# Kernel tuning notes

Hardware: AMD Instinct MI355X
Metric: run time of the kernel (lower is better)

## Reference

```python
import jax, jax.numpy as jnp
import numpy as np

B, N, F_IN, H, FO = 4, 2048, 256, 4, 64


def setup_inputs() -> dict:
    key = jax.random.key(0)
    k1, k2, k3, k4, k5 = jax.random.split(key, 5)
    x = jax.random.normal(k1, (B, N, F_IN), dtype=jnp.float32)
    # random 0/1 adjacency with self-loops so every row of softmax is finite
    adj = jax.random.randint(k2, (N, N), 0, 2).astype(jnp.float32)
    adj = jnp.maximum(adj, jnp.eye(N, dtype=jnp.float32))
    # parameters (xavier-uniform style)
    lim_w = float(np.sqrt(6.0 / (F_IN + H * FO)))
    W = jax.random.uniform(k3, (F_IN, H * FO), minval=-lim_w, maxval=lim_w, dtype=jnp.float32)
    lim_a = float(np.sqrt(6.0 / (H + FO)))
    a_src = jax.random.uniform(k4, (H, FO), minval=-lim_a, maxval=lim_a, dtype=jnp.float32)
    a_dst = jax.random.uniform(k5, (H, FO), minval=-lim_a, maxval=lim_a, dtype=jnp.float32)
    return {"x": x, "adj": adj, "W": W, "a_src": a_src, "a_dst": a_dst}


def reference(x, adj, W, a_src, a_dst):
    # h: (B, N, H, FO)
    h = (x @ W).reshape(B, N, H, FO)
    attn_src = jnp.einsum("bnhf,hf->bnh", h, a_src)  # (B,N,H)
    attn_dst = jnp.einsum("bnhf,hf->bnh", h, a_dst)  # (B,N,H)
    # scores[b,i,j,h] = src[b,i,h] + dst[b,j,h]
    scores = attn_src[:, :, None, :] + attn_dst[:, None, :, :]
    scores = jax.nn.leaky_relu(scores, negative_slope=0.2)
    mask = (adj == 0)[None, :, :, None]  # (1,N,N,1)
    scores = jnp.where(mask, -jnp.inf, scores)
    attn = jax.nn.softmax(scores, axis=2)  # softmax over neighbors j
    # dropout is identity in eval mode / p=0
    out = jnp.einsum("bijh,bjhf->bihf", attn, h)  # (B,N,H,FO)
    return out.reshape(B, N, H * FO)  # concat=True
```

## Files before the change

kernel.cpp:

```cpp
#include <hip/hip_runtime.h>
#include <hip/hip_bf16.h>
#include <math.h>

#define B 4
#define N 2048
#define FIN 256
#define H 4
#define FO 64
#define M (B*N)
#define HF (H*FO)

typedef __attribute__((ext_vector_type(8))) short short8;
typedef __attribute__((ext_vector_type(4))) float float4v;
typedef __attribute__((ext_vector_type(4))) int int4v;

#if __has_builtin(__builtin_amdgcn_exp2f)
#define EXP2(x) __builtin_amdgcn_exp2f(x)
#else
#define EXP2(x) exp2f(x)
#endif

static __device__ __forceinline__ unsigned int pk_rne(float a, float b) {
  unsigned int ua = __builtin_bit_cast(unsigned int, a);
  unsigned int ub = __builtin_bit_cast(unsigned int, b);
  ua += 0x7fffu + ((ua >> 16) & 1u);
  ub += 0x7fffu + ((ub >> 16) & 1u);
  return (ua >> 16) | (ub & 0xffff0000u);
}

static __device__ __forceinline__ unsigned int pk_trunc(float a, float b) {
#if __has_builtin(__builtin_amdgcn_perm)
  return __builtin_amdgcn_perm(__builtin_bit_cast(unsigned int, b),
                               __builtin_bit_cast(unsigned int, a), 0x07060302u);
#else
  return (__builtin_bit_cast(unsigned int, a) >> 16) |
         (__builtin_bit_cast(unsigned int, b) & 0xffff0000u);
#endif
}

static __device__ __forceinline__ void split_pair(float x0, float x1,
                                                  unsigned int& hi, unsigned int& lo) {
  unsigned int u0 = __builtin_bit_cast(unsigned int, x0);
  unsigned int u1 = __builtin_bit_cast(unsigned int, x1);
  hi = (u0 >> 16) | (u1 & 0xffff0000u);
  float h0 = __builtin_bit_cast(float, u0 & 0xffff0000u);
  float h1 = __builtin_bit_cast(float, u1 & 0xffff0000u);
  unsigned int l0 = __builtin_bit_cast(unsigned int, x0 - h0);
  unsigned int l1 = __builtin_bit_cast(unsigned int, x1 - h1);
  lo = (l0 >> 16) | (l1 & 0xffff0000u);
}

static __device__ __forceinline__ unsigned int fenc(float f) {
  unsigned int b = __builtin_bit_cast(unsigned int, f);
  return (b & 0x80000000u) ? ~b : (b | 0x80000000u);
}
static __device__ __forceinline__ float fdec(unsigned int e) {
  unsigned int b = (e & 0x80000000u) ? (e & 0x7fffffffu) : ~e;
  return __builtin_bit_cast(float, b);
}

__global__ __launch_bounds__(256) void prep_wx(const float* __restrict__ Wsrc,
                                               const float* __restrict__ X,
                                               unsigned short* __restrict__ Wf_hi,
                                               unsigned short* __restrict__ Wf_lo,
                                               unsigned short* __restrict__ Xf_hi,
                                               unsigned short* __restrict__ Xf_lo,
                                               unsigned int* __restrict__ DmaxEnc) {
  const int blk = blockIdx.x;
  const int t = threadIdx.x;
  __shared__ float lds[64][65];
  if (blk < 16) {
    if (blk == 0 && t < 16) DmaxEnc[t] = 0u;
    const int k0 = (blk >> 2) * 64;
    const int h  = blk & 3;
    const int n0 = h * 64;
    const int c4 = (t & 15) * 4;
    #pragma unroll
    for (int rep = 0; rep < 4; ++rep) {
      const int kl = (t >> 4) + 16 * rep;
      const float4 v = *(const float4*)(Wsrc + (size_t)(k0 + kl) * HF + n0 + c4);
      lds[kl][c4 + 0] = v.x; lds[kl][c4 + 1] = v.y;
      lds[kl][c4 + 2] = v.z; lds[kl][c4 + 3] = v.w;
    }
    __syncthreads();
    #pragma unroll
    for (int rep = 0; rep < 2; ++rep) {
      const int s   = t + rep * 256;
      const int kcl = s >> 8;
      const int tt  = (s >> 6) & 3;
      const int ln  = s & 63;
      const int fL  = tt * 16 + (ln & 15);
      const int kb  = kcl * 32 + (ln >> 4) * 8;
      unsigned int hv[4], lv[4];
      #pragma unroll
      for (int p = 0; p < 4; ++p)
        split_pair(lds[kb + 2 * p][fL], lds[kb + 2 * p + 1][fL], hv[p], lv[p]);
      const size_t off = ((((size_t)h * 8 + (k0 >> 5) + kcl) * 4 + tt) << 9) + ln * 8;
      *(uint4*)(Wf_hi + off) = make_uint4(hv[0], hv[1], hv[2], hv[3]);
      *(uint4*)(Wf_lo + off) = make_uint4(lv[0], lv[1], lv[2], lv[3]);
    }
    return;
  }
  const int xblk  = blk - 16;
  const int mrow0 = xblk * 64;
  for (int ktile = 0; ktile < 4; ++ktile) {
    if (ktile) __syncthreads();
    const int k0 = ktile * 64;
    const int c4 = (t & 15) * 4;
    #pragma unroll
    for (int rep = 0; rep < 4; ++rep) {
      const int rl = (t >> 4) + 16 * rep;
      const float4 v = *(const float4*)(X + (size_t)(mrow0 + rl) * FIN + k0 + c4);
      lds[rl][c4 + 0] = v.x; lds[rl][c4 + 1] = v.y;
      lds[rl][c4 + 2] = v.z; lds[rl][c4 + 3] = v.w;
    }
    __syncthreads();
    #pragma unroll
    for (int rep = 0; rep < 2; ++rep) {
      const int s   = t + rep * 256;
      const int mt  = s >> 7;
      const int kcl = (s >> 6) & 1;
      const int ln  = s & 63;
      const int mrl = mt * 16 + (ln & 15);
      const int kb  = kcl * 32 + (ln >> 4) * 8;
      unsigned int hv[4], lv[4];
      #pragma unroll
      for (int p = 0; p < 4; ++p)
        split_pair(lds[mrl][kb + 2 * p], lds[mrl][kb + 2 * p + 1], hv[p], lv[p]);
      const size_t off = (((size_t)(xblk * 4 + mt) * 8 + (ktile * 2 + kcl)) << 9) + ln * 8;
      *(uint4*)(Xf_hi + off) = make_uint4(hv[0], hv[1], hv[2], hv[3]);
      *(uint4*)(Xf_lo + off) = make_uint4(lv[0], lv[1], lv[2], lv[3]);
    }
  }
}

__global__ __launch_bounds__(256) void gemm_fused(const unsigned short* __restrict__ Xf_hi,
                                                  const unsigned short* __restrict__ Xf_lo,
                                                  const unsigned short* __restrict__ Wf_hi,
                                                  const unsigned short* __restrict__ Wf_lo,
                                                  const float* __restrict__ adj,
                                                  const float* __restrict__ a_src,
                                                  const float* __restrict__ a_dst,
                                                  float* __restrict__ Srcv,
                                                  float2* __restrict__ Epair,
                                                  unsigned int* __restrict__ DmaxEnc,
                                                  unsigned long long* __restrict__ packed,
                                                  unsigned short* __restrict__ Hf) {
  if (blockIdx.x >= 512) {
    const int row = blockIdx.x - 512;
    const int pw = threadIdx.x >> 6, pl = threadIdx.x & 63;
    const float* ar = adj + (size_t)row * N;
    for (int c = pw; c < N / 64; c += 4) {
      unsigned long long m = __ballot(ar[c * 64 + pl] != 0.f);
      if (pl == 0) packed[(size_t)row * (N / 64) + c] = m;
    }
    return;
  }
  __shared__ unsigned short sh[64][72];
  __shared__ float smax[4];
  const int xcd  = blockIdx.x & 7;
  const int slot = blockIdx.x >> 3;
  const int mb = xcd * 16 + (slot >> 2);
  const int h  = slot & 3;
  const int w = threadIdx.x >> 6, lane = threadIdx.x & 63;
  const int fl = lane & 15, quad = lane >> 4;
  const float L2E = 1.4426950408889634f;

  const float4v zero = {0.f, 0.f, 0.f, 0.f};
  float4v acc[4] = {zero, zero, zero, zero};

  const size_t abase = (((size_t)(mb * 4 + w) * 8) << 9) + lane * 8;
  #pragma unroll
  for (int kc = 0; kc < 8; ++kc) {
    const short8 Ahi = *(const short8*)(Xf_hi + abase + ((size_t)kc << 9));
    const short8 Alo = *(const short8*)(Xf_lo + abase + ((size_t)kc << 9));
    #pragma unroll
    for (int t = 0; t < 4; ++t) {
      const size_t woff = ((((size_t)h * 8 + kc) * 4 + t) << 9) + lane * 8;
      const short8 Bhi = *(const short8*)(Wf_hi + woff);
      const short8 Blo = *(const short8*)(Wf_lo + woff);
      acc[t] = __builtin_amdgcn_mfma_f32_16x16x32_bf16(Ahi, Bhi, acc[t], 0, 0, 0);
      acc[t] = __builtin_amdgcn_mfma_f32_16x16x32_bf16(Alo, Bhi, acc[t], 0, 0, 0);
      acc[t] = __builtin_amdgcn_mfma_f32_16x16x32_bf16(Ahi, Blo, acc[t], 0, 0, 0);
    }
  }

  const int bb  = (mb * 64) >> 11;
  const int n0w = (mb * 64) & (N - 1);
  const int bh  = bb * H + h;
  float as[4], ad[4];
  #pragma unroll
  for (int t = 0; t < 4; ++t) {
    as[t] = a_src[h * FO + t * 16 + fl];
    ad[t] = a_dst[h * FO + t * 16 + fl];
  }
  float wmax = -INFINITY;
  #pragma unroll
  for (int reg = 0; reg < 4; ++reg) {
    float sv = 0.f, dv = 0.f;
    #pragma unroll
    for (int t = 0; t < 4; ++t) {
      sv = fmaf(acc[t][reg], as[t], sv);
      dv = fmaf(acc[t][reg], ad[t], dv);
    }
    #pragma unroll
    for (int off = 1; off <= 8; off <<= 1) {
      sv += __shfl_xor(sv, off, 64);
      dv += __shfl_xor(dv, off, 64);
    }
    wmax = fmaxf(wmax, dv);
    if (fl == 0) {
      const int node = n0w + w * 16 + quad * 4 + reg;
      Srcv[(bh << 11) + node] = sv;
      float2 e;
      e.x = EXP2(dv * L2E);
      e.y = EXP2(dv * (0.2f * L2E));
      Epair[(bh << 11) + node] = e;
    }
  }
  wmax = fmaxf(wmax, __shfl_xor(wmax, 16, 64));
  wmax = fmaxf(wmax, __shfl_xor(wmax, 32, 64));
  if (lane == 0) smax[w] = wmax;

  #pragma unroll
  for (int t = 0; t < 4; ++t) {
    const int nl = w * 16 + quad * 4;
    *(unsigned int*)&sh[t * 16 + fl][nl]     = pk_rne(acc[t][0], acc[t][1]);
    *(unsigned int*)&sh[t * 16 + fl][nl + 2] = pk_rne(acc[t][2], acc[t][3]);
  }
  __syncthreads();
  if (threadIdx.x == 0) {
    const float bmax = fmaxf(fmaxf(smax[0], smax[1]), fmaxf(smax[2], smax[3]));
    atomicMax(DmaxEnc + bh, fenc(bmax));
  }
  const int jc0 = n0w >> 5;
  #pragma unroll
  for (int rep = 0; rep < 2; ++rep) {
    const int s = (int)threadIdx.x + rep * 256;
    const int jcl = s >> 8;
    const int tt  = (s >> 6) & 3;
    const int ln  = s & 63;
    const int f    = tt * 16 + (ln & 15);
    const int node = jcl * 32 + (ln >> 4) * 8;
    unsigned short* dsth = Hf + (((size_t)bh * 64 + jc0 + jcl) * 4 + tt) * 512 + ln * 8;
    *(uint4*)dsth = *(const uint4*)&sh[f][node];
  }
}

__global__ __launch_bounds__(512) void gat_mfma(const unsigned char* __restrict__ pb,
                                                const float* __restrict__ Src,
                                                const float2* __restrict__ Epair,
                                                const unsigned int* __restrict__ DmaxEnc,
                                                const unsigned short* __restrict__ Hf,
                                                float* __restrict__ out) {
  const int xcd  = blockIdx.x & 7;
  const int slot = blockIdx.x >> 3;
  const int b    = xcd >> 1;
  const int i0   = ((xcd & 1) * 32 + slot) * 32;
  const int w    = threadIdx.x >> 6;
  const int lane = threadIdx.x & 63;
  const int h    = w & 3;
  const int jh   = w >> 2;
  const int bh   = b * H + h;
  const int fl   = lane & 15;
  const int kk   = (lane >> 4) * 8;
  const float L2E = 1.4426950408889634f;

  const int row0 = i0 + fl;
  const int row1 = i0 + 16 + fl;
  const float dmx = fdec(DmaxEnc[bh]);
  const float s0 = Src[(bh << 11) + row0];
  const float s1 = Src[(bh << 11) + row1];
  const float u0 = s0 + dmx, m0 = fmaxf(u0, 0.2f * u0);
  const float u1 = s1 + dmx, m1 = fmaxf(u1, 0.2f * u1);
  const float c1a = EXP2((s0 - m0) * L2E), c2a = EXP2((0.2f * s0 - m0) * L2E);
  const float c1b = EXP2((s1 - m1) * L2E), c2b = EXP2((0.2f * s1 - m1) * L2E);
  const float ta = EXP2(-s0 * L2E), tb = EXP2(-s1 * L2E);
  const float* ep = (const float*)(Epair + (bh << 11));
  const unsigned char* pb0 = pb + (size_t)row0 * (N / 8);
  const unsigned char* pb1 = pb + (size_t)row1 * (N / 8);
  const unsigned short* hfb = Hf + (size_t)bh * 64 * 2048 + lane * 8;

  const short onebf = 0x3F80;
  short8 ones;
  #pragma unroll
  for (int jj = 0; jj < 8; ++jj) ones[jj] = onebf;

  const float4v zero = {0.f, 0.f, 0.f, 0.f};
  float4v acc[2][4];
  float4v accL[2];
  #pragma unroll
  for (int rt = 0; rt < 2; ++rt) {
    accL[rt] = zero;
    #pragma unroll
    for (int t = 0; t < 4; ++t) acc[rt][t] = zero;
  }

  const int jbeg = jh * (N / 2);
  short8 nb0, nb1, nb2, nb3;
  float4 nq0, nq1, nq2, nq3;
  unsigned int nm0, nm1;
  {
    const unsigned short* hc = hfb + (size_t)(jbeg >> 5) * 2048;
    nb0 = *(const short8*)(hc + 0 * 512);
    nb1 = *(const short8*)(hc + 1 * 512);
    nb2 = *(const short8*)(hc + 2 * 512);
    nb3 = *(const short8*)(hc + 3 * 512);
    nq0 = *(const float4*)(ep + 2 * (jbeg + kk) + 0);
    nq1 = *(const float4*)(ep + 2 * (jbeg + kk) + 4);
    nq2 = *(const float4*)(ep + 2 * (jbeg + kk) + 8);
    nq3 = *(const float4*)(ep + 2 * (jbeg + kk) + 12);
    nm0 = pb0[(jbeg + kk) >> 3];
    nm1 = pb1[(jbeg + kk) >> 3];
  }

  for (int it = 0; it < 32; ++it) {
    const short8 b0 = nb0, b1 = nb1, b2 = nb2, b3 = nb3;
    const float4 q0 = nq0, q1 = nq1, q2 = nq2, q3 = nq3;
    const unsigned int mk0 = nm0, mk1 = nm1;
    if (it < 31) {
      const int jn = jbeg + (it + 1) * 32;
      const unsigned short* hc = hfb + (size_t)(jn >> 5) * 2048;
      nb0 = *(const short8*)(hc + 0 * 512);
      nb1 = *(const short8*)(hc + 1 * 512);
      nb2 = *(const short8*)(hc + 2 * 512);
      nb3 = *(const short8*)(hc + 3 * 512);
      nq0 = *(const float4*)(ep + 2 * (jn + kk) + 0);
      nq1 = *(const float4*)(ep + 2 * (jn + kk) + 4);
      nq2 = *(const float4*)(ep + 2 * (jn + kk) + 8);
      nq3 = *(const float4*)(ep + 2 * (jn + kk) + 12);
      nm0 = pb0[(jn + kk) >> 3];
      nm1 = pb1[(jn + kk) >> 3];
    }
    const float E1v[8] = {q0.x, q0.z, q1.x, q1.z, q2.x, q2.z, q3.x, q3.z};
    const float E2v[8] = {q0.y, q0.w, q1.y, q1.w, q2.y, q2.w, q3.y, q3.w};
    int p0i[4], p1i[4];
    #pragma unroll
    for (int p = 0; p < 4; ++p) {
      const int e0 = 2 * p, e1 = 2 * p + 1;
      const bool sa0 = E1v[e0] > ta;
      float va0 = (sa0 ? c1a : c2a) * (sa0 ? E1v[e0] : E2v[e0]);
      va0 = ((mk0 >> e0) & 1u) ? va0 : 0.f;
      const bool sa1 = E1v[e1] > ta;
      float va1 = (sa1 ? c1a : c2a) * (sa1 ? E1v[e1] : E2v[e1]);
      va1 = ((mk0 >> e1) & 1u) ? va1 : 0.f;
      p0i[p] = (int)pk_trunc(va0, va1);
      const bool sb0 = E1v[e0] > tb;
      float vb0 = (sb0 ? c1b : c2b) * (sb0 ? E1v[e0] : E2v[e0]);
      vb0 = ((mk1 >> e0) & 1u) ? vb0 : 0.f;
      const bool sb1 = E1v[e1] > tb;
      float vb1 = (sb1 ? c1b : c2b) * (sb1 ? E1v[e1] : E2v[e1]);
      vb1 = ((mk1 >> e1) & 1u) ? vb1 : 0.f;
      p1i[p] = (int)pk_trunc(vb0, vb1);
    }
    const short8 p0 = __builtin_bit_cast(short8, (int4v){p0i[0], p0i[1], p0i[2], p0i[3]});
    const short8 p1 = __builtin_bit_cast(short8, (int4v){p1i[0], p1i[1], p1i[2], p1i[3]});
    acc[0][0] = __builtin_amdgcn_mfma_f32_16x16x32_bf16(p0, b0, acc[0][0], 0, 0, 0);
    acc[0][1] = __builtin_amdgcn_mfma_f32_16x16x32_bf16(p0, b1, acc[0][1], 0, 0, 0);
    acc[0][2] = __builtin_amdgcn_mfma_f32_16x16x32_bf16(p0, b2, acc[0][2], 0, 0, 0);
    acc[0][3] = __builtin_amdgcn_mfma_f32_16x16x32_bf16(p0, b3, acc[0][3], 0, 0, 0);
    accL[0]   = __builtin_amdgcn_mfma_f32_16x16x32_bf16(p0, ones, accL[0], 0, 0, 0);
    acc[1][0] = __builtin_amdgcn_mfma_f32_16x16x32_bf16(p1, b0, acc[1][0], 0, 0, 0);
    acc[1][1] = __builtin_amdgcn_mfma_f32_16x16x32_bf16(p1, b1, acc[1][1], 0, 0, 0);
    acc[1][2] = __builtin_amdgcn_mfma_f32_16x16x32_bf16(p1, b2, acc[1][2], 0, 0, 0);
    acc[1][3] = __builtin_amdgcn_mfma_f32_16x16x32_bf16(p1, b3, acc[1][3], 0, 0, 0);
    accL[1]   = __builtin_amdgcn_mfma_f32_16x16x32_bf16(p1, ones, accL[1], 0, 0, 0);
  }

  __shared__ float4v parts[4][64][11];
  if (jh == 1) {
    #pragma unroll
    for (int rt = 0; rt < 2; ++rt) {
      #pragma unroll
      for (int t = 0; t < 4; ++t) parts[h][lane][rt * 5 + t] = acc[rt][t];
      parts[h][lane][rt * 5 + 4] = accL[rt];
    }
  }
  __syncthreads();
  if (jh == 0) {
    #pragma unroll
    for (int rt = 0; rt < 2; ++rt) {
      #pragma unroll
      for (int t = 0; t < 4; ++t) acc[rt][t] += parts[h][lane][rt * 5 + t];
      accL[rt] += parts[h][lane][rt * 5 + 4];
    }
    const int quad = lane >> 4;
    #pragma unroll
    for (int rt = 0; rt < 2; ++rt) {
      #pragma unroll
      for (int reg = 0; reg < 4; ++reg) {
        const int r = i0 + rt * 16 + quad * 4 + reg;
        const float invl = 1.f / accL[rt][reg];
        float* op = out + ((size_t)(b * N) + r) * HF + h * FO + fl;
        #pragma unroll
        for (int t = 0; t < 4; ++t) op[t * 16] = acc[rt][t][reg] * invl;
      }
    }
  }
}

extern "C" void kernel_launch(void* const* d_in, const int* in_sizes, int n_in,
                              void* d_out, int out_size, void* d_ws, size_t ws_size,
                              hipStream_t stream) {
  const float* x     = (const float*)d_in[0];
  const float* adj   = (const float*)d_in[1];
  const float* W     = (const float*)d_in[2];
  const float* a_src = (const float*)d_in[3];
  const float* a_dst = (const float*)d_in[4];
  float* out = (float*)d_out;

  char* p = (char*)d_ws;
  float* Srcv = (float*)p;                 p += (size_t)B * H * N * 4;
  float2* Epair = (float2*)p;              p += (size_t)B * H * N * 8;
  unsigned int* DmaxEnc = (unsigned int*)p; p += 256;
  unsigned short* Wfh = (unsigned short*)p; p += (size_t)HF * FIN * 2;
  unsigned short* Wfl = (unsigned short*)p; p += (size_t)HF * FIN * 2;
  unsigned short* Xfh = (unsigned short*)p; p += (size_t)M * FIN * 2;
  unsigned short* Xfl = (unsigned short*)p; p += (size_t)M * FIN * 2;
  unsigned short* Hf  = (unsigned short*)p; p += (size_t)M * HF * 2;
  unsigned long long* packed = (unsigned long long*)p;

  prep_wx<<<dim3(144), dim3(256), 0, stream>>>(W, x, Wfh, Wfl, Xfh, Xfl, DmaxEnc);
  gemm_fused<<<dim3(512 + N), dim3(256), 0, stream>>>(Xfh, Xfl, Wfh, Wfl, adj,
                                                      a_src, a_dst,
                                                      Srcv, Epair, DmaxEnc,
                                                      packed, Hf);
  gat_mfma<<<dim3(B * (N / 32)), dim3(512), 0, stream>>>((const unsigned char*)packed,
                                                         Srcv, Epair, DmaxEnc, Hf, out);
}
```

Measured before the change: 127.1 us.

## Store adjacency bitmask transposed so mask byte loads coalesce across rows

The adjacency packing blocks now handle 16 rows each, staging the ballot bitmasks in shared memory and writing them out transposed (byte-column major: packT[colbyte][row]). In the attention kernel, the lanes that load mask bytes for consecutive rows now read contiguous bytes instead of addresses strided by 256 bytes, which is meant to reduce scattered global loads in the inner loop. The packing grid shrinks from 2048 to 128 blocks, so each block does 16x the ballot work, which may lengthen that phase if it is on the critical path.

```diff
diff --git a/kernel.cpp b/kernel.cpp
--- a/kernel.cpp
+++ b/kernel.cpp
@@ -144,16 +144,27 @@
                                                   float* __restrict__ Srcv,
                                                   float2* __restrict__ Epair,
                                                   unsigned int* __restrict__ DmaxEnc,
-                                                  unsigned long long* __restrict__ packed,
+                                                  unsigned char* __restrict__ packT,
                                                   unsigned short* __restrict__ Hf) {
   if (blockIdx.x >= 512) {
-    const int row = blockIdx.x - 512;
+    __shared__ unsigned char lb[16][256];
+    const int r0 = (blockIdx.x - 512) * 16;
     const int pw = threadIdx.x >> 6, pl = threadIdx.x & 63;
-    const float* ar = adj + (size_t)row * N;
-    for (int c = pw; c < N / 64; c += 4) {
-      unsigned long long m = __ballot(ar[c * 64 + pl] != 0.f);
-      if (pl == 0) packed[(size_t)row * (N / 64) + c] = m;
-    }
+    for (int rr = pw; rr < 16; rr += 4) {
+      const float* ar = adj + (size_t)(r0 + rr) * N;
+      for (int c = 0; c < N / 64; ++c) {
+        unsigned long long m = __ballot(ar[c * 64 + pl] != 0.f);
+        if (pl == 0) *(unsigned long long*)&lb[rr][c * 8] = m;
+      }
+    }
+    __syncthreads();
+    const int t = threadIdx.x;
+    unsigned int wv[4];
+    #pragma unroll
+    for (int g = 0; g < 4; ++g)
+      wv[g] = (unsigned int)lb[4 * g + 0][t] | ((unsigned int)lb[4 * g + 1][t] << 8)
+            | ((unsigned int)lb[4 * g + 2][t] << 16) | ((unsigned int)lb[4 * g + 3][t] << 24);
+    *(uint4*)(packT + (size_t)t * 2048 + r0) = make_uint4(wv[0], wv[1], wv[2], wv[3]);
     return;
   }
   __shared__ unsigned short sh[64][72];
@@ -247,7 +258,7 @@
   }
 }
 
-__global__ __launch_bounds__(512) void gat_mfma(const unsigned char* __restrict__ pb,
+__global__ __launch_bounds__(512) void gat_mfma(const unsigned char* __restrict__ pT,
                                                 const float* __restrict__ Src,
                                                 const float2* __restrict__ Epair,
                                                 const unsigned int* __restrict__ DmaxEnc,
@@ -277,8 +288,6 @@
   const float c1b = EXP2((s1 - m1) * L2E), c2b = EXP2((0.2f * s1 - m1) * L2E);
   const float ta = EXP2(-s0 * L2E), tb = EXP2(-s1 * L2E);
   const float* ep = (const float*)(Epair + (bh << 11));
-  const unsigned char* pb0 = pb + (size_t)row0 * (N / 8);
-  const unsigned char* pb1 = pb + (size_t)row1 * (N / 8);
   const unsigned short* hfb = Hf + (size_t)bh * 64 * 2048 + lane * 8;
 
   const short onebf = 0x3F80;
@@ -310,8 +319,9 @@
     nq1 = *(const float4*)(ep + 2 * (jbeg + kk) + 4);
     nq2 = *(const float4*)(ep + 2 * (jbeg + kk) + 8);
     nq3 = *(const float4*)(ep + 2 * (jbeg + kk) + 12);
-    nm0 = pb0[(jbeg + kk) >> 3];
-    nm1 = pb1[(jbeg + kk) >> 3];
+    const size_t bc = (size_t)((jbeg + kk) >> 3) << 11;
+    nm0 = pT[bc + row0];
+    nm1 = pT[bc + row1];
   }
 
   for (int it = 0; it < 32; ++it) {
@@ -329,8 +339,9 @@
       nq1 = *(const float4*)(ep + 2 * (jn + kk) + 4);
       nq2 = *(const float4*)(ep + 2 * (jn + kk) + 8);
       nq3 = *(const float4*)(ep + 2 * (jn + kk) + 12);
-      nm0 = pb0[(jn + kk) >> 3];
-      nm1 = pb1[(jn + kk) >> 3];
+      const size_t bc = (size_t)((jn + kk) >> 3) << 11;
+      nm0 = pT[bc + row0];
+      nm1 = pT[bc + row1];
     }
     const float E1v[8] = {q0.x, q0.z, q1.x, q1.z, q2.x, q2.z, q3.x, q3.z};
     const float E2v[8] = {q0.y, q0.w, q1.y, q1.w, q2.y, q2.w, q3.y, q3.w};
@@ -418,13 +429,13 @@
   unsigned short* Xfh = (unsigned short*)p; p += (size_t)M * FIN * 2;
   unsigned short* Xfl = (unsigned short*)p; p += (size_t)M * FIN * 2;
   unsigned short* Hf  = (unsigned short*)p; p += (size_t)M * HF * 2;
-  unsigned long long* packed = (unsigned long long*)p;
+  unsigned char* packT = (unsigned char*)p;
 
   prep_wx<<<dim3(144), dim3(256), 0, stream>>>(W, x, Wfh, Wfl, Xfh, Xfl, DmaxEnc);
-  gemm_fused<<<dim3(512 + N), dim3(256), 0, stream>>>(Xfh, Xfl, Wfh, Wfl, adj,
-                                                      a_src, a_dst,
-                                                      Srcv, Epair, DmaxEnc,
-                                                      packed, Hf);
-  gat_mfma<<<dim3(B * (N / 32)), dim3(512), 0, stream>>>((const unsigned char*)packed,
+  gemm_fused<<<dim3(512 + 128), dim3(256), 0, stream>>>(Xfh, Xfl, Wfh, Wfl, adj,
+                                                        a_src, a_dst,
+                                                        Srcv, Epair, DmaxEnc,
+                                                        packT, Hf);
+  gat_mfma<<<dim3(B * (N / 32)), dim3(512), 0, stream>>>(packT,
                                                          Srcv, Epair, DmaxEnc, Hf, out);
 }
```

Measured after the change: 149.4 us. 17.5% more time.
